# Kernel tuning notes

Measured on AMD Instinct MI355X. Metric: run time of the kernel, lower is better.

The kernel has to match this reference:

```python
import jax, jax.numpy as jnp
import numpy as np

EMBED = 1024
TOKLEN = 100
NLAYERS = 24
TOKDIM = 256
MLP = int(EMBED * 0.125)  # 128, hardcoded mlp_ratio=0.125
SEQ, BATCH = 4097, 8  # 4096 patch tokens + 1 cls token


def setup_inputs() -> dict:
    key = jax.random.key(0)
    ks = jax.random.split(key, 8)
    s = 0.02  # kaiming-like small init scale
    return {
        "x": jax.random.normal(ks[0], (SEQ, BATCH, EMBED), jnp.float32),
        "layer": 3,
        "A": jax.random.normal(ks[1], (1, TOKLEN, EMBED), jnp.float32) * s,
        "B": jax.random.normal(ks[2], (NLAYERS, EMBED, TOKDIM), jnp.float32) * s,
        "Wd": jax.random.normal(ks[3], (MLP, TOKDIM), jnp.float32) * s,
        "bd": jnp.zeros((MLP,), jnp.float32),
        "Wu": jax.random.normal(ks[4], (EMBED, MLP), jnp.float32) * s,
        "bu": jnp.zeros((EMBED,), jnp.float32),
        "Wt": jax.random.normal(ks[5], (EMBED, EMBED), jnp.float32) * s,
        "bt": jnp.zeros((EMBED,), jnp.float32),
        "Wf": jax.random.normal(ks[6], (EMBED, EMBED), jnp.float32) * s,
        "bf": jnp.zeros((EMBED,), jnp.float32),
        "scale": jnp.asarray(0.001, jnp.float32),
    }


def reference(x, layer, A, B, Wd, bd, Wu, bu, Wt, bt, Wf, bf, scale):
    # batch_first=False, has_cls_token=True, evp_feature=None (module defaults)
    cls_tok, body = x[:1], x[1:]              # [1,b,c], [n,b,c]
    # get_tokens(layer): tokens = A[0] @ up(gelu(down(B[layer])))
    Bl = B[layer]                              # [c, token_dim]
    fB = jax.nn.gelu(Bl @ Wd.T + bd, approximate=False) @ Wu.T + bu  # [c, c]
    tokens = A[0] @ fB                         # [m, c]
    # forward_delta_feat: cross-attention to the m=100 learned tokens
    attn = jax.nn.softmax(
        jnp.einsum("nbc,mc->nbm", body, tokens) * (EMBED ** -0.5), axis=-1
    )                                          # [n, b, m]
    tfeat = tokens @ Wt.T + bt                 # mlp_token2feat, [m, c]
    delta = jnp.einsum("nbm,mc->nbc", attn, tfeat)
    delta = (delta + body) @ Wf.T + bf         # mlp_delta_f
    out = body + delta * scale                 # scaled residual fuse
    return jnp.concatenate([cls_tok, out], axis=0)
```

## Files before the change

kernel.cpp:

```cpp
#include <hip/hip_runtime.h>
#include <stdint.h>

#define EMBED 1024
#define TOKLEN 100
#define TOKDIM 256
#define MLPD 128
#define KEXT 1152

typedef float f32x4 __attribute__((ext_vector_type(4)));
typedef __bf16 bf16x8 __attribute__((ext_vector_type(8)));

__device__ __forceinline__ unsigned short f2bf(float f) {
  unsigned int u = __float_as_uint(f);
  u += 0x7fffu + ((u >> 16) & 1);
  return (unsigned short)(u >> 16);
}
__device__ __forceinline__ float bf2f(unsigned short h) {
  return __uint_as_float(((unsigned int)h) << 16);
}
__device__ __forceinline__ void async16(const void* g, void* l) {
  __builtin_amdgcn_global_load_lds(
      (const __attribute__((address_space(1))) unsigned int*)g,
      (__attribute__((address_space(3))) unsigned int*)l, 16, 0, 0);
}



__global__ void k_gelu(const float* __restrict__ B, const int* __restrict__ layer,
                       const float* __restrict__ Wd, const float* __restrict__ bd,
                       float* __restrict__ G) {
  int idx = blockIdx.x * 256 + threadIdx.x;
  int c = idx >> 7, j = idx & 127;
  const float* bl = B + ((size_t)layer[0] * EMBED + c) * TOKDIM;
  const float* wd = Wd + (size_t)j * TOKDIM;
  float a0 = 0.f, a1 = 0.f, a2 = 0.f, a3 = 0.f;
  for (int k = 0; k < TOKDIM; k += 4) {
    float4 a = *(const float4*)(bl + k);
    float4 b = *(const float4*)(wd + k);
    a0 += a.x * b.x; a1 += a.y * b.y; a2 += a.z * b.z; a3 += a.w * b.w;
  }
  float v = a0 + a1 + a2 + a3 + bd[j];
  G[idx] = 0.5f * v * (1.f + erff(v * 0.70710678118654752440f));
}

__global__ void k_ag(const float* __restrict__ A, const float* __restrict__ G,
                     float* __restrict__ AG, float* __restrict__ asum) {
  int m = blockIdx.x, j = threadIdx.x;
  const float* a = A + (size_t)m * EMBED;
  float acc = 0.f, s = 0.f;
  for (int c = 0; c < EMBED; ++c) acc += a[c] * G[(size_t)c * MLPD + j];
  AG[(size_t)m * MLPD + j] = acc;
  for (int c = j; c < EMBED; c += 128) s += a[c];
  __shared__ float red[128];
  red[j] = s; __syncthreads();
  for (int w = 64; w > 0; w >>= 1) { if (j < w) red[j] += red[j + w]; __syncthreads(); }
  if (j == 0) asum[m] = red[0];
}

__global__ void k_tokens(const float* __restrict__ AG, const float* __restrict__ asum,
                         const float* __restrict__ Wu, const float* __restrict__ bu,
                         unsigned short* __restrict__ tokbf) {
  int m = blockIdx.x, t = threadIdx.x;
  if (m >= TOKLEN) {
    #pragma unroll
    for (int i = 0; i < 4; ++i) tokbf[(size_t)m * EMBED + t * 4 + i] = 0;
    return;
  }
  __shared__ float ag[MLPD];
  __shared__ float as_s;
  if (t < MLPD) ag[t] = AG[(size_t)m * MLPD + t];
  if (t == 0) as_s = asum[m];
  __syncthreads();
  #pragma unroll
  for (int i = 0; i < 4; ++i) {
    int e = t * 4 + i;
    const float* wu = Wu + (size_t)e * MLPD;
    float a0 = 0.f, a1 = 0.f, a2 = 0.f, a3 = 0.f;
    for (int j = 0; j < MLPD; j += 4) {
      float4 w = *(const float4*)(wu + j);
      a0 += w.x * ag[j]; a1 += w.y * ag[j + 1]; a2 += w.z * ag[j + 2]; a3 += w.w * ag[j + 3];
    }
    tokbf[(size_t)m * EMBED + e] = f2bf(a0 + a1 + a2 + a3 + as_s * bu[e]);
  }
}

__global__ void k_wprep(const float* __restrict__ Wf, const float* __restrict__ Wt,
                        const float* __restrict__ bt,
                        unsigned short* __restrict__ Bt, unsigned short* __restrict__ wfbf,
                        unsigned short* __restrict__ wtbf, float* __restrict__ wfbt) {
  int e = blockIdx.x, t = threadIdx.x;
  float4 v = *(const float4*)(Wf + (size_t)e * EMBED + t * 4);
  uint2 u;
  u.x = (unsigned int)f2bf(v.x) | ((unsigned int)f2bf(v.y) << 16);
  u.y = (unsigned int)f2bf(v.z) | ((unsigned int)f2bf(v.w) << 16);
  *(uint2*)(Bt + (size_t)e * KEXT + t * 4) = u;
  *(uint2*)(wfbf + (size_t)e * EMBED + t * 4) = u;
  if (t < 28) Bt[(size_t)e * KEXT + 1124 + t] = 0;
  float4 w = *(const float4*)(Wt + (size_t)e * EMBED + t * 4);
  uint2 u2;
  u2.x = (unsigned int)f2bf(w.x) | ((unsigned int)f2bf(w.y) << 16);
  u2.y = (unsigned int)f2bf(w.z) | ((unsigned int)f2bf(w.w) << 16);
  *(uint2*)(wtbf + (size_t)e * EMBED + t * 4) = u2;
  float4 b = *(const float4*)(bt + t * 4);
  __shared__ float red[256];
  red[t] = v.x * b.x + v.y * b.y + v.z * b.z + v.w * b.w;
  __syncthreads();
  for (int s = 128; s > 0; s >>= 1) { if (t < s) red[t] += red[t + s]; __syncthreads(); }
  if (t == 0) wfbt[e] = red[0];
}

__global__ void k_cls(const float* __restrict__ x, float* __restrict__ out) {
  int i = blockIdx.x * 256 + threadIdx.x;
  ((float4*)out)[i] = ((const float4*)x)[i];
}


__global__ void __launch_bounds__(256) k_tf1(const unsigned short* __restrict__ tokbf,
                                             const unsigned short* __restrict__ wtbf,
                                             unsigned short* __restrict__ tfeatbf) {
  __shared__ unsigned short As[2][128 * 64];
  __shared__ unsigned short Bs[2][128 * 64];
  const int tid = threadIdx.x;
  const int wave = tid >> 6, lane = tid & 63;
  const int l15 = lane & 15, quad = lane >> 4;
  const int srow = lane >> 3, schunk = lane & 7;
  const int col0 = blockIdx.x * 128;
  const int wr = (wave >> 1) * 64, wc = (wave & 1) * 64;

  f32x4 acc[4][4];
  const f32x4 zero = {0.f, 0.f, 0.f, 0.f};
  #pragma unroll
  for (int i = 0; i < 4; ++i)
    #pragma unroll
    for (int j = 0; j < 4; ++j) acc[i][j] = zero;

  auto stage = [&](int buf, int kt) {
    const int k0 = kt * 64;
    #pragma unroll
    for (int i = 0; i < 4; ++i) {
      const int r = i * 32 + wave * 8;
      async16(tokbf + (size_t)(r + srow) * EMBED + k0 + (schunk ^ srow) * 8, &As[buf][r * 64]);
      async16(wtbf + (size_t)(col0 + r + srow) * EMBED + k0 + (schunk ^ srow) * 8, &Bs[buf][r * 64]);
    }
  };
  auto compute = [&](int buf) {
    #pragma unroll
    for (int ks = 0; ks < 2; ++ks) {
      const int sw = ((ks * 4 + quad) ^ (l15 & 7)) * 8;
      bf16x8 a[4], b[4];
      #pragma unroll
      for (int i = 0; i < 4; ++i)
        a[i] = *(const bf16x8*)&As[buf][(wr + i * 16 + l15) * 64 + sw];
      #pragma unroll
      for (int j = 0; j < 4; ++j)
        b[j] = *(const bf16x8*)&Bs[buf][(wc + j * 16 + l15) * 64 + sw];
      #pragma unroll
      for (int i = 0; i < 4; ++i)
        #pragma unroll
        for (int j = 0; j < 4; ++j)
          acc[i][j] = __builtin_amdgcn_mfma_f32_16x16x32_bf16(a[i], b[j], acc[i][j], 0, 0, 0);
    }
  };

  stage(0, 0);
  asm volatile("s_waitcnt vmcnt(0)" ::: "memory");
  __syncthreads();
  int cur = 0;
  for (int kt = 0; kt < 16; ++kt) {
    if (kt < 15) stage(cur ^ 1, kt + 1);
    compute(cur);
    asm volatile("s_waitcnt vmcnt(0)" ::: "memory");
    __syncthreads();
    cur ^= 1;
  }
  #pragma unroll
  for (int j = 0; j < 4; ++j) {
    const int e = col0 + wc + j * 16 + l15;
    #pragma unroll
    for (int i = 0; i < 4; ++i) {
      const int mb = wr + i * 16 + quad * 4;
      #pragma unroll
      for (int r = 0; r < 4; ++r)
        tfeatbf[(size_t)(mb + r) * EMBED + e] = f2bf(acc[i][j][r]);
    }
  }
}

__global__ void __launch_bounds__(256) k_tf2(const unsigned short* __restrict__ wfbf,
                                             const unsigned short* __restrict__ tfeatbf,
                                             const float* __restrict__ wfbt,
                                             unsigned short* __restrict__ Bt) {
  __shared__ unsigned short As[2][128 * 64];
  __shared__ unsigned short Bs[2][128 * 64];
  const int tid = threadIdx.x;
  const int wave = tid >> 6, lane = tid & 63;
  const int l15 = lane & 15, quad = lane >> 4;
  const int srow = lane >> 3, schunk = lane & 7;
  const int row0 = blockIdx.x * 128;
  const int wr = (wave >> 1) * 64, wc = (wave & 1) * 64;

  f32x4 acc[4][4];
  const f32x4 zero = {0.f, 0.f, 0.f, 0.f};
  #pragma unroll
  for (int i = 0; i < 4; ++i)
    #pragma unroll
    for (int j = 0; j < 4; ++j) acc[i][j] = zero;

  auto stage = [&](int buf, int kt) {
    const int k0 = kt * 64;
    #pragma unroll
    for (int i = 0; i < 4; ++i) {
      const int r = i * 32 + wave * 8;
      async16(wfbf + (size_t)(row0 + r + srow) * EMBED + k0 + (schunk ^ srow) * 8, &As[buf][r * 64]);
      async16(tfeatbf + (size_t)(r + srow) * EMBED + k0 + (schunk ^ srow) * 8, &Bs[buf][r * 64]);
    }
  };
  auto compute = [&](int buf) {
    #pragma unroll
    for (int ks = 0; ks < 2; ++ks) {
      const int sw = ((ks * 4 + quad) ^ (l15 & 7)) * 8;
      bf16x8 a[4], b[4];
      #pragma unroll
      for (int i = 0; i < 4; ++i)
        a[i] = *(const bf16x8*)&As[buf][(wr + i * 16 + l15) * 64 + sw];
      #pragma unroll
      for (int j = 0; j < 4; ++j)
        b[j] = *(const bf16x8*)&Bs[buf][(wc + j * 16 + l15) * 64 + sw];
      #pragma unroll
      for (int i = 0; i < 4; ++i)
        #pragma unroll
        for (int j = 0; j < 4; ++j)
          acc[i][j] = __builtin_amdgcn_mfma_f32_16x16x32_bf16(a[i], b[j], acc[i][j], 0, 0, 0);
    }
  };

  stage(0, 0);
  asm volatile("s_waitcnt vmcnt(0)" ::: "memory");
  __syncthreads();
  int cur = 0;
  for (int kt = 0; kt < 16; ++kt) {
    if (kt < 15) stage(cur ^ 1, kt + 1);
    compute(cur);
    asm volatile("s_waitcnt vmcnt(0)" ::: "memory");
    __syncthreads();
    cur ^= 1;
  }
  #pragma unroll
  for (int j = 0; j < 4; ++j) {
    const int m = wc + j * 16 + l15;
    #pragma unroll
    for (int i = 0; i < 4; ++i) {
      const int eb = row0 + wr + i * 16 + quad * 4;
      #pragma unroll
      for (int r = 0; r < 4; ++r)
        Bt[(size_t)(eb + r) * KEXT + 1024 + m] = f2bf(acc[i][j][r] + wfbt[eb + r]);
    }
  }
}

__global__ void __launch_bounds__(256) k_attn(const float* __restrict__ x,
                                              const unsigned short* __restrict__ tokbf,
                                              unsigned short* __restrict__ Aext) {
  __shared__ __align__(16) unsigned short smem[2 * 128 * 72 + 2 * 128 * 64];
  const int tid = threadIdx.x;
  const int wave = tid >> 6, lane = tid & 63;
  const int l15 = lane & 15, quad = lane >> 4;
  const int srow = lane >> 3, schunk = lane & 7;
  const int row0 = blockIdx.x * 128;
  const int trow = tid >> 1, thalf = tid & 1;
  const float* body = x + 8 * EMBED;
  const float* gxbase = body + (size_t)(row0 + trow) * EMBED + thalf * 32;

  f32x4 acc[2][8];
  const f32x4 zero = {0.f, 0.f, 0.f, 0.f};
  #pragma unroll
  for (int i = 0; i < 2; ++i)
    #pragma unroll
    for (int j = 0; j < 8; ++j) acc[i][j] = zero;

  float4 v[8];

  auto regload = [&](int kt) {
    const float* gx = gxbase + kt * 64;
    #pragma unroll
    for (int q = 0; q < 8; ++q) v[q] = *(const float4*)(gx + q * 4);
  };
  auto tsstage = [&](int buf, int kt) {
    unsigned short* Ts = smem + 2 * 128 * 72 + buf * (128 * 64);
    const int k0 = kt * 64;
    #pragma unroll
    for (int i = 0; i < 4; ++i) {
      const int r = i * 32 + wave * 8;
      async16(tokbf + (size_t)(r + srow) * EMBED + k0 + (schunk ^ srow) * 8, &Ts[r * 64]);
    }
  };
  auto convwrite = [&](int buf, int kt) {
    unsigned short* As = smem + buf * (128 * 72);
    unsigned int pk[16];
    #pragma unroll
    for (int q = 0; q < 8; ++q) {
      pk[q * 2]     = (unsigned int)f2bf(v[q].x) | ((unsigned int)f2bf(v[q].y) << 16);
      pk[q * 2 + 1] = (unsigned int)f2bf(v[q].z) | ((unsigned int)f2bf(v[q].w) << 16);
    }
    unsigned int* lw = (unsigned int*)&As[trow * 72 + thalf * 32];
    unsigned int* gw = (unsigned int*)(Aext + (size_t)(row0 + trow) * KEXT + kt * 64 + thalf * 32);
    #pragma unroll
    for (int q = 0; q < 4; ++q) {
      uint4 u; u.x = pk[q*4]; u.y = pk[q*4+1]; u.z = pk[q*4+2]; u.w = pk[q*4+3];
      ((uint4*)lw)[q] = u;
      ((uint4*)gw)[q] = u;
    }
  };
  auto compute = [&](int buf) {
    unsigned short* As = smem + buf * (128 * 72);
    unsigned short* Ts = smem + 2 * 128 * 72 + buf * (128 * 64);
    #pragma unroll
    for (int ks = 0; ks < 2; ++ks) {
      const int sw = ((ks * 4 + quad) ^ (l15 & 7)) * 8;
      bf16x8 a[2], b[8];
      #pragma unroll
      for (int i = 0; i < 2; ++i)
        a[i] = *(const bf16x8*)&As[(wave * 32 + i * 16 + l15) * 72 + ks * 32 + quad * 8];
      #pragma unroll
      for (int j = 0; j < 8; ++j)
        b[j] = *(const bf16x8*)&Ts[(j * 16 + l15) * 64 + sw];
      #pragma unroll
      for (int i = 0; i < 2; ++i)
        #pragma unroll
        for (int j = 0; j < 8; ++j)
          acc[i][j] = __builtin_amdgcn_mfma_f32_16x16x32_bf16(a[i], b[j], acc[i][j], 0, 0, 0);
    }
  };

  regload(0); tsstage(0, 0);
  asm volatile("s_waitcnt vmcnt(0)" ::: "memory");
  convwrite(0, 0);
  __syncthreads();
  int cur = 0;
  for (int kt = 0; kt < 16; ++kt) {
    if (kt < 15) { regload(kt + 1); tsstage(cur ^ 1, kt + 1); }
    compute(cur);
    if (kt < 15) {
      asm volatile("s_waitcnt vmcnt(0)" ::: "memory");
      convwrite(cur ^ 1, kt + 1);
    }
    __syncthreads();
    cur ^= 1;
  }

  unsigned short* Sc = smem;
  #pragma unroll
  for (int i = 0; i < 2; ++i) {
    #pragma unroll
    for (int r = 0; r < 4; ++r) {
      float mx = -1e30f;
      #pragma unroll
      for (int j = 0; j < 8; ++j) {
        const int c = j * 16 + l15;
        const float vv = acc[i][j][r] * 0.03125f;
        if (c < TOKLEN) mx = fmaxf(mx, vv);
      }
      #pragma unroll
      for (int d = 1; d < 16; d <<= 1) mx = fmaxf(mx, __shfl_xor(mx, d));
      float sm = 0.f;
      #pragma unroll
      for (int j = 0; j < 8; ++j) {
        const int c = j * 16 + l15;
        if (c < TOKLEN) sm += __expf(acc[i][j][r] * 0.03125f - mx);
      }
      #pragma unroll
      for (int d = 1; d < 16; d <<= 1) sm += __shfl_xor(sm, d);
      const float inv = 1.f / sm;
      const int row = wave * 32 + i * 16 + quad * 4 + r;
      #pragma unroll
      for (int j = 0; j < 8; ++j) {
        const int c = j * 16 + l15;
        const float p = (c < TOKLEN) ? __expf(acc[i][j][r] * 0.03125f - mx) * inv : 0.f;
        Sc[row * 128 + c] = f2bf(p);
      }
    }
  }
  __syncthreads();
  {
    const int r = tid >> 1, h = tid & 1;
    const uint4* src = (const uint4*)(Sc + r * 128 + h * 64);
    uint4* dst = (uint4*)(Aext + (size_t)(row0 + r) * KEXT + 1024 + h * 64);
    dst[0] = src[0]; dst[1] = src[1]; dst[2] = src[2]; dst[3] = src[3];
  }
}

__global__ void __launch_bounds__(256) k_main(const unsigned short* __restrict__ Aext,
                                              const unsigned short* __restrict__ Bt,
                                              const float* __restrict__ x,
                                              const float* __restrict__ bfv,
                                              const float* __restrict__ scale,
                                              float* __restrict__ out) {
  __shared__ unsigned short As[2][128 * 64];
  __shared__ unsigned short Bs[2][128 * 64];
  const int tid = threadIdx.x;
  const int wave = tid >> 6, lane = tid & 63;
  const int l15 = lane & 15, quad = lane >> 4;
  const int srow = lane >> 3, schunk = lane & 7;
  const int xcd = blockIdx.x & 7, slot = blockIdx.x >> 3;
  const int row0 = ((slot >> 3) * 8 + xcd) * 128;
  const int col0 = (slot & 7) * 128;
  const int wr = (wave >> 1) * 64, wc = (wave & 1) * 64;

  f32x4 acc[4][4];
  const f32x4 zero = {0.f, 0.f, 0.f, 0.f};
  #pragma unroll
  for (int i = 0; i < 4; ++i)
    #pragma unroll
    for (int j = 0; j < 4; ++j) acc[i][j] = zero;

  auto stage = [&](int buf, int kt) {
    const int k0 = kt * 64;
    #pragma unroll
    for (int i = 0; i < 4; ++i) {
      const int r = i * 32 + wave * 8;
      async16(Aext + (size_t)(row0 + r + srow) * KEXT + k0 + (schunk ^ srow) * 8, &As[buf][r * 64]);
      async16(Bt   + (size_t)(col0 + r + srow) * KEXT + k0 + (schunk ^ srow) * 8, &Bs[buf][r * 64]);
    }
  };
  auto compute = [&](int buf) {
    #pragma unroll
    for (int ks = 0; ks < 2; ++ks) {
      const int sw = ((ks * 4 + quad) ^ (l15 & 7)) * 8;
      bf16x8 a[4], b[4];
      #pragma unroll
      for (int i = 0; i < 4; ++i)
        a[i] = *(const bf16x8*)&As[buf][(wr + i * 16 + l15) * 64 + sw];
      #pragma unroll
      for (int j = 0; j < 4; ++j)
        b[j] = *(const bf16x8*)&Bs[buf][(wc + j * 16 + l15) * 64 + sw];
      #pragma unroll
      for (int i = 0; i < 4; ++i)
        #pragma unroll
        for (int j = 0; j < 4; ++j)
          acc[i][j] = __builtin_amdgcn_mfma_f32_16x16x32_bf16(a[i], b[j], acc[i][j], 0, 0, 0);
    }
  };

  stage(0, 0);
  asm volatile("s_waitcnt vmcnt(0)" ::: "memory");
  __syncthreads();
  int cur = 0;
  for (int kt = 0; kt < 18; ++kt) {
    if (kt < 17) stage(cur ^ 1, kt + 1);
    compute(cur);
    asm volatile("s_waitcnt vmcnt(0)" ::: "memory");
    __syncthreads();
    cur ^= 1;
  }

  const float s = scale[0];
  #pragma unroll
  for (int j = 0; j < 4; ++j) {
    const int c = col0 + wc + j * 16 + l15;
    const float bfc = bfv[c];
    #pragma unroll
    for (int i = 0; i < 4; ++i) {
      const int rb = row0 + wr + i * 16 + quad * 4;
      #pragma unroll
      for (int r = 0; r < 4; ++r) {
        const size_t idx = (size_t)(rb + r + 8) * EMBED + c;
        out[idx] = x[idx] + (acc[i][j][r] + bfc) * s;
      }
    }
  }
}

extern "C" void kernel_launch(void* const* d_in, const int* in_sizes, int n_in,
                              void* d_out, int out_size, void* d_ws, size_t ws_size,
                              hipStream_t stream) {
  const float* x     = (const float*)d_in[0];
  const int*   layer = (const int*)d_in[1];
  const float* A     = (const float*)d_in[2];
  const float* B     = (const float*)d_in[3];
  const float* Wd    = (const float*)d_in[4];
  const float* bd    = (const float*)d_in[5];
  const float* Wu    = (const float*)d_in[6];
  const float* bu    = (const float*)d_in[7];
  const float* Wt    = (const float*)d_in[8];
  const float* bt    = (const float*)d_in[9];
  const float* Wf    = (const float*)d_in[10];
  const float* bf    = (const float*)d_in[11];
  const float* scale = (const float*)d_in[12];
  float* out = (float*)d_out;

  char* ws = (char*)d_ws;
  unsigned short* Aext    = (unsigned short*)(ws + 0);
  unsigned short* wtbf    = (unsigned short*)(ws + 0);
  unsigned short* wfbf    = (unsigned short*)(ws + 2097152);
  unsigned short* Bt_     = (unsigned short*)(ws + 75497472);
  unsigned short* tokbf   = (unsigned short*)(ws + 77856768);
  float*          G       = (float*)(ws + 78118912);
  float*          AG      = (float*)(ws + 78643200);
  float*          asum    = (float*)(ws + 78694400);
  float*          wfbt    = (float*)(ws + 78694912);
  unsigned short* tfeatbf = (unsigned short*)(ws + 78699008);

  k_gelu  <<<512, 256, 0, stream>>>(B, layer, Wd, bd, G);
  k_ag    <<<100, 128, 0, stream>>>(A, G, AG, asum);
  k_tokens<<<128, 256, 0, stream>>>(AG, asum, Wu, bu, tokbf);
  k_wprep <<<1024, 256, 0, stream>>>(Wf, Wt, bt, Bt_, wfbf, wtbf, wfbt);
  k_tf1   <<<8, 256, 0, stream>>>(tokbf, wtbf, tfeatbf);
  k_tf2   <<<8, 256, 0, stream>>>(wfbf, tfeatbf, wfbt, Bt_);
  k_cls   <<<8, 256, 0, stream>>>(x, out);
  k_attn  <<<256, 256, 0, stream>>>(x, tokbf, Aext);
  k_main  <<<2048, 256, 0, stream>>>(Aext, Bt_, x, bf, scale, out);
}
```

Baseline: 538.8 us.

## Enlarge main GEMM tile to 256x256 with 8 waves and phased MFMA scheduling

The main fused GEMM moves from 128x128 tiles with 4 waves to 256x256 tiles with 8 waves and 512 threads per block. The K loop is unrolled by two over double buffers and split into sub-phases that load LDS fragments, hit a barrier, then issue MFMAs at raised priority (setprio). The aim is less global/L2 traffic per FLOP and better overlap of memory and matrix work across waves. In exchange it uses 128KB of LDS and more accumulator registers, so occupancy may drop, and the extra barriers add sync overhead.

```diff
diff --git a/kernel.cpp b/kernel.cpp
--- a/kernel.cpp
+++ b/kernel.cpp
@@ -389,82 +389,122 @@
   }
 }
 
-__global__ void __launch_bounds__(256) k_main(const unsigned short* __restrict__ Aext,
+
+#define MAIN_PHASE(S, MH, NH)                                                   \
+  do {                                                                          \
+    bf16x8 pa0, pa1, pa2, pa3, pb0, pb1, pa4, pa5, pa6, pa7, pb2, pb3;          \
+    {                                                                           \
+      const int sw0 = ((0 * 4 + quad) ^ (l15 & 7)) * 8;                         \
+      const int sw1 = ((1 * 4 + quad) ^ (l15 & 7)) * 8;                         \
+      const unsigned short* Ah = &Ab[S][wm][0];                                 \
+      const unsigned short* Bh = &Bb[S][bh][0];                                 \
+      pa0 = *(const bf16x8*)&Ah[((MH)*64 + 0*16 + l15) * 64 + sw0];             \
+      pa1 = *(const bf16x8*)&Ah[((MH)*64 + 1*16 + l15) * 64 + sw0];             \
+      pa2 = *(const bf16x8*)&Ah[((MH)*64 + 2*16 + l15) * 64 + sw0];             \
+      pa3 = *(const bf16x8*)&Ah[((MH)*64 + 3*16 + l15) * 64 + sw0];             \
+      pb0 = *(const bf16x8*)&Bh[(brb + (NH)*32 + 0*16 + l15) * 64 + sw0];       \
+      pb1 = *(const bf16x8*)&Bh[(brb + (NH)*32 + 1*16 + l15) * 64 + sw0];       \
+      pa4 = *(const bf16x8*)&Ah[((MH)*64 + 0*16 + l15) * 64 + sw1];             \
+      pa5 = *(const bf16x8*)&Ah[((MH)*64 + 1*16 + l15) * 64 + sw1];             \
+      pa6 = *(const bf16x8*)&Ah[((MH)*64 + 2*16 + l15) * 64 + sw1];             \
+      pa7 = *(const bf16x8*)&Ah[((MH)*64 + 3*16 + l15) * 64 + sw1];             \
+      pb2 = *(const bf16x8*)&Bh[(brb + (NH)*32 + 0*16 + l15) * 64 + sw1];       \
+      pb3 = *(const bf16x8*)&Bh[(brb + (NH)*32 + 1*16 + l15) * 64 + sw1];       \
+    }                                                                           \
+    asm volatile("s_barrier" ::: "memory");                                     \
+    __builtin_amdgcn_s_setprio(1);                                              \
+    acc[(MH)*4+0][(NH)*2+0] = __builtin_amdgcn_mfma_f32_16x16x32_bf16(pa0, pb0, acc[(MH)*4+0][(NH)*2+0], 0, 0, 0); \
+    acc[(MH)*4+1][(NH)*2+0] = __builtin_amdgcn_mfma_f32_16x16x32_bf16(pa1, pb0, acc[(MH)*4+1][(NH)*2+0], 0, 0, 0); \
+    acc[(MH)*4+2][(NH)*2+0] = __builtin_amdgcn_mfma_f32_16x16x32_bf16(pa2, pb0, acc[(MH)*4+2][(NH)*2+0], 0, 0, 0); \
+    acc[(MH)*4+3][(NH)*2+0] = __builtin_amdgcn_mfma_f32_16x16x32_bf16(pa3, pb0, acc[(MH)*4+3][(NH)*2+0], 0, 0, 0); \
+    acc[(MH)*4+0][(NH)*2+1] = __builtin_amdgcn_mfma_f32_16x16x32_bf16(pa0, pb1, acc[(MH)*4+0][(NH)*2+1], 0, 0, 0); \
+    acc[(MH)*4+1][(NH)*2+1] = __builtin_amdgcn_mfma_f32_16x16x32_bf16(pa1, pb1, acc[(MH)*4+1][(NH)*2+1], 0, 0, 0); \
+    acc[(MH)*4+2][(NH)*2+1] = __builtin_amdgcn_mfma_f32_16x16x32_bf16(pa2, pb1, acc[(MH)*4+2][(NH)*2+1], 0, 0, 0); \
+    acc[(MH)*4+3][(NH)*2+1] = __builtin_amdgcn_mfma_f32_16x16x32_bf16(pa3, pb1, acc[(MH)*4+3][(NH)*2+1], 0, 0, 0); \
+    acc[(MH)*4+0][(NH)*2+0] = __builtin_amdgcn_mfma_f32_16x16x32_bf16(pa4, pb2, acc[(MH)*4+0][(NH)*2+0], 0, 0, 0); \
+    acc[(MH)*4+1][(NH)*2+0] = __builtin_amdgcn_mfma_f32_16x16x32_bf16(pa5, pb2, acc[(MH)*4+1][(NH)*2+0], 0, 0, 0); \
+    acc[(MH)*4+2][(NH)*2+0] = __builtin_amdgcn_mfma_f32_16x16x32_bf16(pa6, pb2, acc[(MH)*4+2][(NH)*2+0], 0, 0, 0); \
+    acc[(MH)*4+3][(NH)*2+0] = __builtin_amdgcn_mfma_f32_16x16x32_bf16(pa7, pb2, acc[(MH)*4+3][(NH)*2+0], 0, 0, 0); \
+    acc[(MH)*4+0][(NH)*2+1] = __builtin_amdgcn_mfma_f32_16x16x32_bf16(pa4, pb3, acc[(MH)*4+0][(NH)*2+1], 0, 0, 0); \
+    acc[(MH)*4+1][(NH)*2+1] = __builtin_amdgcn_mfma_f32_16x16x32_bf16(pa5, pb3, acc[(MH)*4+1][(NH)*2+1], 0, 0, 0); \
+    acc[(MH)*4+2][(NH)*2+1] = __builtin_amdgcn_mfma_f32_16x16x32_bf16(pa6, pb3, acc[(MH)*4+2][(NH)*2+1], 0, 0, 0); \
+    acc[(MH)*4+3][(NH)*2+1] = __builtin_amdgcn_mfma_f32_16x16x32_bf16(pa7, pb3, acc[(MH)*4+3][(NH)*2+1], 0, 0, 0); \
+    __builtin_amdgcn_s_setprio(0);                                              \
+    asm volatile("s_barrier" ::: "memory");                                     \
+  } while (0)
+
+#define ISSUE_TILE(KT, S)                                                       \
+  do {                                                                          \
+    const int k0_ = (KT) * 64;                                                  \
+    _Pragma("unroll")                                                           \
+    for (int h_ = 0; h_ < 2; ++h_) {                                            \
+      _Pragma("unroll")                                                         \
+      for (int r2_ = 0; r2_ < 2; ++r2_) {                                       \
+        const int rb_ = r2_ * 64 + w8;                                          \
+        async16(Aext + (size_t)(row0 + h_ * 128 + rb_ + srow) * KEXT + k0_ + (schunk ^ srow) * 8, \
+                &Ab[S][h_][rb_ * 64]);                                          \
+        async16(Bt + (size_t)(col0 + h_ * 128 + rb_ + srow) * KEXT + k0_ + (schunk ^ srow) * 8,   \
+                &Bb[S][h_][rb_ * 64]);                                          \
+      }                                                                         \
+    }                                                                           \
+  } while (0)
+
+__global__ void __launch_bounds__(512) k_main(const unsigned short* __restrict__ Aext,
                                               const unsigned short* __restrict__ Bt,
                                               const float* __restrict__ x,
                                               const float* __restrict__ bfv,
                                               const float* __restrict__ scale,
                                               float* __restrict__ out) {
-  __shared__ unsigned short As[2][128 * 64];
-  __shared__ unsigned short Bs[2][128 * 64];
+  __shared__ unsigned short Ab[2][2][128 * 64];
+  __shared__ unsigned short Bb[2][2][128 * 64];
   const int tid = threadIdx.x;
-  const int wave = tid >> 6, lane = tid & 63;
+  const int w = tid >> 6, lane = tid & 63;
   const int l15 = lane & 15, quad = lane >> 4;
   const int srow = lane >> 3, schunk = lane & 7;
+  const int w8 = w * 8;
+  const int wm = w >> 2, wn = w & 3;
+  const int bh = wn >> 1, brb = (wn & 1) * 64;
+
   const int xcd = blockIdx.x & 7, slot = blockIdx.x >> 3;
-  const int row0 = ((slot >> 3) * 8 + xcd) * 128;
-  const int col0 = (slot & 7) * 128;
-  const int wr = (wave >> 1) * 64, wc = (wave & 1) * 64;
-
-  f32x4 acc[4][4];
+  const int rt = (slot >> 2) * 8 + xcd;
+  const int ct = slot & 3;
+  const int row0 = rt * 256;
+  const int col0 = ct * 256;
+
+  f32x4 acc[8][4];
   const f32x4 zero = {0.f, 0.f, 0.f, 0.f};
   #pragma unroll
-  for (int i = 0; i < 4; ++i)
+  for (int i = 0; i < 8; ++i)
     #pragma unroll
     for (int j = 0; j < 4; ++j) acc[i][j] = zero;
 
-  auto stage = [&](int buf, int kt) {
-    const int k0 = kt * 64;
-    #pragma unroll
-    for (int i = 0; i < 4; ++i) {
-      const int r = i * 32 + wave * 8;
-      async16(Aext + (size_t)(row0 + r + srow) * KEXT + k0 + (schunk ^ srow) * 8, &As[buf][r * 64]);
-      async16(Bt   + (size_t)(col0 + r + srow) * KEXT + k0 + (schunk ^ srow) * 8, &Bs[buf][r * 64]);
-    }
-  };
-  auto compute = [&](int buf) {
-    #pragma unroll
-    for (int ks = 0; ks < 2; ++ks) {
-      const int sw = ((ks * 4 + quad) ^ (l15 & 7)) * 8;
-      bf16x8 a[4], b[4];
-      #pragma unroll
-      for (int i = 0; i < 4; ++i)
-        a[i] = *(const bf16x8*)&As[buf][(wr + i * 16 + l15) * 64 + sw];
-      #pragma unroll
-      for (int j = 0; j < 4; ++j)
-        b[j] = *(const bf16x8*)&Bs[buf][(wc + j * 16 + l15) * 64 + sw];
-      #pragma unroll
-      for (int i = 0; i < 4; ++i)
-        #pragma unroll
-        for (int j = 0; j < 4; ++j)
-          acc[i][j] = __builtin_amdgcn_mfma_f32_16x16x32_bf16(a[i], b[j], acc[i][j], 0, 0, 0);
-    }
-  };
-
-  stage(0, 0);
-  asm volatile("s_waitcnt vmcnt(0)" ::: "memory");
-  __syncthreads();
-  int cur = 0;
-  for (int kt = 0; kt < 18; ++kt) {
-    if (kt < 17) stage(cur ^ 1, kt + 1);
-    compute(cur);
+  ISSUE_TILE(0, 0);
+  #pragma unroll 1
+  for (int i = 0; i < 9; ++i) {
     asm volatile("s_waitcnt vmcnt(0)" ::: "memory");
-    __syncthreads();
-    cur ^= 1;
+    asm volatile("s_barrier" ::: "memory");
+    ISSUE_TILE(2 * i + 1, 1);
+    MAIN_PHASE(0, 0, 0); MAIN_PHASE(0, 0, 1);
+    MAIN_PHASE(0, 1, 0); MAIN_PHASE(0, 1, 1);
+    asm volatile("s_waitcnt vmcnt(0)" ::: "memory");
+    asm volatile("s_barrier" ::: "memory");
+    if (i < 8) ISSUE_TILE(2 * i + 2, 0);
+    MAIN_PHASE(1, 0, 0); MAIN_PHASE(1, 0, 1);
+    MAIN_PHASE(1, 1, 0); MAIN_PHASE(1, 1, 1);
   }
 
   const float s = scale[0];
   #pragma unroll
-  for (int j = 0; j < 4; ++j) {
-    const int c = col0 + wc + j * 16 + l15;
-    const float bfc = bfv[c];
-    #pragma unroll
-    for (int i = 0; i < 4; ++i) {
-      const int rb = row0 + wr + i * 16 + quad * 4;
+  for (int mf = 0; mf < 8; ++mf) {
+    const int rb = row0 + wm * 128 + mf * 16 + quad * 4;
+    #pragma unroll
+    for (int nf = 0; nf < 4; ++nf) {
+      const int c = col0 + wn * 64 + nf * 16 + l15;
+      const float bfc = bfv[c];
       #pragma unroll
       for (int r = 0; r < 4; ++r) {
         const size_t idx = (size_t)(rb + r + 8) * EMBED + c;
-        out[idx] = x[idx] + (acc[i][j][r] + bfc) * s;
+        out[idx] = x[idx] + (acc[mf][nf][r] + bfc) * s;
       }
     }
   }
@@ -508,5 +548,5 @@
   k_tf2   <<<8, 256, 0, stream>>>(wfbf, tfeatbf, wfbt, Bt_);
   k_cls   <<<8, 256, 0, stream>>>(x, out);
   k_attn  <<<256, 256, 0, stream>>>(x, tokbf, Aext);
-  k_main  <<<2048, 256, 0, stream>>>(Aext, Bt_, x, bf, scale, out);
-}
+  k_main  <<<512, 512, 0, stream>>>(Aext, Bt_, x, bf, scale, out);
+}
```

Measured after the change: 542.3 us. About the same (+0.6%).
